# Performance work log

Measured on AMD Instinct MI355X. Metric: run time of the kernel, lower is better.

The kernel has to match this reference:

```python
import jax, jax.numpy as jnp
import numpy as np

N_NODES = 100000
IN_DIM = 64
OUT_DIM = 64
N_EDGES = 1250000


def setup_inputs() -> dict:
    key = jax.random.key(0)
    k1, k2, k3, k4 = jax.random.split(key, 4)
    x = jax.random.normal(k1, (N_NODES, IN_DIM), dtype=jnp.float32)
    edge_index = jax.random.randint(k2, (2, N_EDGES), 0, N_NODES, dtype=jnp.int32)
    # Linear weights stored as [in, out] so y = x @ W (equivalent to torch x @ W.T)
    s = 1.0 / np.sqrt(IN_DIM)
    W1 = jax.random.uniform(k3, (IN_DIM, OUT_DIM), dtype=jnp.float32, minval=-s, maxval=s)
    W2 = jax.random.uniform(k4, (IN_DIM, OUT_DIM), dtype=jnp.float32, minval=-s, maxval=s)
    return {"x": x, "edge_index": edge_index, "W1": W1, "W2": W2}


def reference(x, edge_index, W1, W2):
    # self part: [N, out]
    self_part = x @ W1
    # transform-then-gather is mathematically identical to gather-then-transform
    # (linear map commutes with row gather) and cheaper when E > N.
    msgs = (x @ W2)[edge_index[0]]            # [E, out]
    neighbor_part = jax.ops.segment_sum(msgs, edge_index[1], num_segments=x.shape[0])
    return jax.nn.relu(self_part + neighbor_part)
```

## Files before the change

kernel.cpp:

```cpp
#include <hip/hip_runtime.h>

#define N_NODES 100000
#define N_EDGES 1250000
#define DIM 64

#define B_SHIFT 7
#define BUCKET_NODES 128
#define NBUCKETS ((N_NODES + BUCKET_NODES - 1) / BUCKET_NODES)
#define CAP 2560
#define P_CHUNK 4096
#define P_THREADS 512
#define NBLK_P ((N_EDGES + P_CHUNK - 1) / P_CHUNK)
#define GEMM_BLOCKS 512
#define SG_THREADS 1024

typedef __attribute__((ext_vector_type(8))) short short8;
typedef __attribute__((ext_vector_type(4))) float f32x4;

static __host__ __device__ inline size_t align256(size_t x) { return (x + 255) & ~(size_t)255; }

__device__ inline float bf16_to_f32(unsigned short u) {
  return __uint_as_float(((unsigned)u) << 16);
}
__device__ inline unsigned short f32_to_bf16(float f) {
  unsigned u = __float_as_uint(f);
  u += 0x7FFFu + ((u >> 16) & 1u);
  return (unsigned short)(u >> 16);
}

__global__ __launch_bounds__(P_THREADS) void partition_sorted(
    const int* __restrict__ ei,
    int* __restrict__ gcursor,
    unsigned* __restrict__ pairs) {
  __shared__ int h[NBUCKETS];
  __shared__ int scn[NBUCKETS];
  __shared__ int cur[NBUCKETS];
  __shared__ int gbase[NBUCKETS];
  __shared__ int tsum[P_THREADS];
  __shared__ unsigned sval[P_CHUNK];
  __shared__ int saddr[P_CHUNK];

  const int nE = N_EDGES;
  int tid = threadIdx.x;
  int base = blockIdx.x * P_CHUNK;
  int end = min(base + P_CHUNK, nE);
  int cntE = end - base;

  for (int i = tid; i < NBUCKETS; i += P_THREADS) h[i] = 0;
  __syncthreads();
  for (int e = base + tid; e < end; e += P_THREADS)
    atomicAdd(&h[ei[nE + e] >> B_SHIFT], 1);
  __syncthreads();

  {
    int b0 = tid * 2;
    int l0 = 0, l1 = 0, s = 0;
    if (b0 < NBUCKETS)     { l0 = s; s += h[b0]; }
    if (b0 + 1 < NBUCKETS) { l1 = s; s += h[b0 + 1]; }
    tsum[tid] = s;
    __syncthreads();
    for (int off = 1; off < P_THREADS; off <<= 1) {
      int t = (tid >= off) ? tsum[tid - off] : 0;
      __syncthreads();
      tsum[tid] += t;
      __syncthreads();
    }
    int p = tsum[tid] - s;
    if (b0 < NBUCKETS)     scn[b0] = p + l0;
    if (b0 + 1 < NBUCKETS) scn[b0 + 1] = p + l1;
  }
  __syncthreads();

  for (int i = tid; i < NBUCKETS; i += P_THREADS) {
    int c = h[i];
    gbase[i] = c ? atomicAdd(&gcursor[i], c) : 0;
    cur[i] = scn[i];
  }
  __syncthreads();

  for (int e = base + tid; e < end; e += P_THREADS) {
    int dst = ei[nE + e];
    int src = ei[e];
    int b = dst >> B_SHIFT;
    int lp = atomicAdd(&cur[b], 1);
    int inb = lp - scn[b];
    int gpos = gbase[b] + inb;
    sval[lp] = (unsigned)src | ((unsigned)(dst & (BUCKET_NODES - 1)) << 17);
    saddr[lp] = (gpos < CAP) ? (b * CAP + gpos) : -1;
  }
  __syncthreads();

  for (int j = tid; j < cntE; j += P_THREADS) {
    int a = saddr[j];
    if (a >= 0) pairs[a] = sval[j];
  }
}

__global__ __launch_bounds__(256) void gemm_mfma(
    const float* __restrict__ x,
    const float* __restrict__ W1,
    const float* __restrict__ W2,
    unsigned short* __restrict__ y1b,
    unsigned short* __restrict__ y2b,
    int nTiles) {
  int lane = threadIdx.x & 63;
  int wave = (blockIdx.x * 256 + (int)threadIdx.x) >> 6;
  int nWaves = GEMM_BLOCKS * 4;
  int m = lane & 15;
  int q = lane >> 4;

  short8 wf[2][2][4];
#pragma unroll
  for (int w = 0; w < 2; ++w) {
    const float* W = w ? W2 : W1;
#pragma unroll
    for (int kh = 0; kh < 2; ++kh)
#pragma unroll
      for (int nt = 0; nt < 4; ++nt) {
        short8 f;
#pragma unroll
        for (int j = 0; j < 8; ++j) {
          int k = kh * 32 + q * 8 + j;
          f[j] = (short)f32_to_bf16(W[k * DIM + nt * 16 + m]);
        }
        wf[w][kh][nt] = f;
      }
  }

  for (int t = wave; t < nTiles; t += nWaves) {
    int rowBase = t * 16;
    const float* xr = x + (size_t)(rowBase + m) * DIM + q * 8;

    short8 af[2];
#pragma unroll
    for (int kh = 0; kh < 2; ++kh) {
      float4 u0 = *(const float4*)(xr + kh * 32);
      float4 u1 = *(const float4*)(xr + kh * 32 + 4);
      short8 f;
      f[0] = (short)f32_to_bf16(u0.x);
      f[1] = (short)f32_to_bf16(u0.y);
      f[2] = (short)f32_to_bf16(u0.z);
      f[3] = (short)f32_to_bf16(u0.w);
      f[4] = (short)f32_to_bf16(u1.x);
      f[5] = (short)f32_to_bf16(u1.y);
      f[6] = (short)f32_to_bf16(u1.z);
      f[7] = (short)f32_to_bf16(u1.w);
      af[kh] = f;
    }

#pragma unroll
    for (int w = 0; w < 2; ++w) {
      unsigned short* Y = w ? y2b : y1b;
      f32x4 acc[4];
#pragma unroll
      for (int nt = 0; nt < 4; ++nt) {
        acc[nt] = (f32x4){0.f, 0.f, 0.f, 0.f};
        acc[nt] = __builtin_amdgcn_mfma_f32_16x16x32_bf16(af[0], wf[w][0][nt], acc[nt], 0, 0, 0);
        acc[nt] = __builtin_amdgcn_mfma_f32_16x16x32_bf16(af[1], wf[w][1][nt], acc[nt], 0, 0, 0);
      }
#pragma unroll
      for (int nt = 0; nt < 4; ++nt)
#pragma unroll
        for (int r = 0; r < 4; ++r)
          Y[(size_t)(rowBase + q * 4 + r) * DIM + nt * 16 + m] = f32_to_bf16(acc[nt][r]);
    }
  }
}

__global__ __launch_bounds__(SG_THREADS) void sort_gather(
    const unsigned* __restrict__ pairs,
    const int* __restrict__ gcursor,
    const unsigned short* __restrict__ y1b,
    const unsigned short* __restrict__ y2b,
    float* __restrict__ out,
    int nNodesTotal) {
  __shared__ unsigned buf[CAP];
  __shared__ unsigned sorted[CAP];
  __shared__ int cnt[BUCKET_NODES];
  __shared__ int scn[BUCKET_NODES];
  __shared__ int cur[BUCKET_NODES];

  int b = blockIdx.x;
  int n = min(gcursor[b], CAP);
  int tid = threadIdx.x;
  const unsigned* pb = pairs + (size_t)b * CAP;

  if (tid < BUCKET_NODES) cnt[tid] = 0;
  __syncthreads();
  for (int i = tid; i < n; i += SG_THREADS) {
    unsigned w = pb[i];
    buf[i] = w;
    atomicAdd(&cnt[(w >> 17) & 127], 1);
  }
  __syncthreads();

  int v = 0;
  if (tid < BUCKET_NODES) { v = cnt[tid]; scn[tid] = v; }
  __syncthreads();
#pragma unroll
  for (int off = 1; off < BUCKET_NODES; off <<= 1) {
    int t = 0;
    if (tid < BUCKET_NODES && tid >= off) t = scn[tid - off];
    __syncthreads();
    if (tid < BUCKET_NODES) scn[tid] += t;
    __syncthreads();
  }
  if (tid < BUCKET_NODES) cur[tid] = scn[tid] - v;
  __syncthreads();

  for (int i = tid; i < n; i += SG_THREADS) {
    unsigned w = buf[i];
    int l = (int)((w >> 17) & 127);
    int p = atomicAdd(&cur[l], 1);
    sorted[p] = w & 0x1FFFFu;
  }
  __syncthreads();

  int lane = tid & 63;
  int wv = tid >> 6;
  int g = lane >> 4;
  int c16 = lane & 15;
  const ushort4* y2q = (const ushort4*)y2b;
  const ushort4* y1q = (const ushort4*)y1b;
  int nodeBase = b << B_SHIFT;
  int numNodes = min(BUCKET_NODES, nNodesTotal - nodeBase);

  for (int ln = wv; ln < numNodes; ln += (SG_THREADS / 64)) {
    int deg = cnt[ln];
    int begin = scn[ln] - deg;
    int end = begin + deg;

    float ax = 0.f, ay = 0.f, az = 0.f, aw = 0.f;
    float bx = 0.f, by = 0.f, bz = 0.f, bw = 0.f;
    int e = begin;
    for (; e + 7 < end; e += 8) {
      int s0 = (int)sorted[e + g];
      int s1 = (int)sorted[e + 4 + g];
      ushort4 u0 = y2q[(size_t)s0 * 16 + c16];
      ushort4 u1 = y2q[(size_t)s1 * 16 + c16];
      ax += bf16_to_f32(u0.x); ay += bf16_to_f32(u0.y);
      az += bf16_to_f32(u0.z); aw += bf16_to_f32(u0.w);
      bx += bf16_to_f32(u1.x); by += bf16_to_f32(u1.y);
      bz += bf16_to_f32(u1.z); bw += bf16_to_f32(u1.w);
    }
    for (; e + 3 < end; e += 4) {
      int s = (int)sorted[e + g];
      ushort4 u = y2q[(size_t)s * 16 + c16];
      ax += bf16_to_f32(u.x); ay += bf16_to_f32(u.y);
      az += bf16_to_f32(u.z); aw += bf16_to_f32(u.w);
    }
    if (e + g < end) {
      int s = (int)sorted[e + g];
      ushort4 u = y2q[(size_t)s * 16 + c16];
      ax += bf16_to_f32(u.x); ay += bf16_to_f32(u.y);
      az += bf16_to_f32(u.z); aw += bf16_to_f32(u.w);
    }

    float sx = ax + bx, sy = ay + by, sz = az + bz, sw = aw + bw;
    sx += __shfl_xor(sx, 16, 64);
    sy += __shfl_xor(sy, 16, 64);
    sz += __shfl_xor(sz, 16, 64);
    sw += __shfl_xor(sw, 16, 64);
    sx += __shfl_xor(sx, 32, 64);
    sy += __shfl_xor(sy, 32, 64);
    sz += __shfl_xor(sz, 32, 64);
    sw += __shfl_xor(sw, 32, 64);

    if (lane < 16) {
      int node = nodeBase + ln;
      ushort4 s1v = y1q[(size_t)node * 16 + lane];
      float4 o;
      o.x = fmaxf(bf16_to_f32(s1v.x) + sx, 0.0f);
      o.y = fmaxf(bf16_to_f32(s1v.y) + sy, 0.0f);
      o.z = fmaxf(bf16_to_f32(s1v.z) + sz, 0.0f);
      o.w = fmaxf(bf16_to_f32(s1v.w) + sw, 0.0f);
      ((float4*)out)[(size_t)node * 16 + lane] = o;
    }
  }
}

__global__ __launch_bounds__(256) void gemm_simple(
    const float* __restrict__ x, const float* __restrict__ W1, const float* __restrict__ W2,
    float* __restrict__ y1, unsigned short* __restrict__ y2b, int n) {
  int row = blockIdx.x * blockDim.x + threadIdx.x;
  if (row >= n) return;
  float xv[DIM];
  const float4* xr = (const float4*)(x + (size_t)row * DIM);
#pragma unroll
  for (int i = 0; i < DIM / 4; ++i) {
    float4 t = xr[i];
    xv[4 * i] = t.x; xv[4 * i + 1] = t.y; xv[4 * i + 2] = t.z; xv[4 * i + 3] = t.w;
  }
#pragma unroll
  for (int m = 0; m < 2; ++m) {
    const float* W = (m == 0) ? W1 : W2;
#pragma unroll
    for (int cc = 0; cc < DIM; cc += 16) {
      float acc[16];
#pragma unroll
      for (int c2 = 0; c2 < 16; ++c2) acc[c2] = 0.0f;
      for (int k = 0; k < DIM; ++k) {
        float xk = xv[k];
        const float* wr = W + k * DIM + cc;
#pragma unroll
        for (int c2 = 0; c2 < 16; ++c2) acc[c2] = fmaf(xk, wr[c2], acc[c2]);
      }
      if (m == 0) {
        for (int c2 = 0; c2 < 16; ++c2) y1[(size_t)row * DIM + cc + c2] = acc[c2];
      } else {
        for (int c2 = 0; c2 < 16; ++c2) y2b[(size_t)row * DIM + cc + c2] = f32_to_bf16(acc[c2]);
      }
    }
  }
}

__global__ __launch_bounds__(256) void scatter_add(const int* __restrict__ ei,
                                                   const unsigned short* __restrict__ y2b,
                                                   float* __restrict__ out, int nE) {
  int gid = blockIdx.x * blockDim.x + threadIdx.x;
  int edge = gid >> 6;
  int lane = threadIdx.x & 63;
  if (edge >= nE) return;
  int src = __builtin_amdgcn_readfirstlane(ei[edge]);
  int dst = __builtin_amdgcn_readfirstlane(ei[nE + edge]);
  atomicAdd(&out[(size_t)dst * DIM + lane], bf16_to_f32(y2b[(size_t)src * DIM + lane]));
}

__global__ __launch_bounds__(256) void relu_inplace(float* __restrict__ out, int n4) {
  int i = blockIdx.x * blockDim.x + threadIdx.x;
  if (i >= n4) return;
  float4* p = (float4*)out;
  float4 v = p[i];
  v.x = fmaxf(v.x, 0.0f);
  v.y = fmaxf(v.y, 0.0f);
  v.z = fmaxf(v.z, 0.0f);
  v.w = fmaxf(v.w, 0.0f);
  p[i] = v;
}

extern "C" void kernel_launch(void* const* d_in, const int* in_sizes, int n_in,
                              void* d_out, int out_size, void* d_ws, size_t ws_size,
                              hipStream_t stream) {
  const float* x  = (const float*)d_in[0];
  const int*   ei = (const int*)d_in[1];
  const float* W1 = (const float*)d_in[2];
  const float* W2 = (const float*)d_in[3];
  float* out = (float*)d_out;

  char* ws = (char*)d_ws;
  size_t off = 0;
  unsigned short* y2b = (unsigned short*)(ws + off); off += align256((size_t)N_NODES * DIM * sizeof(unsigned short));
  unsigned short* y1b = (unsigned short*)(ws + off); off += align256((size_t)N_NODES * DIM * sizeof(unsigned short));
  int* gcursor = (int*)(ws + off);                   off += align256((size_t)NBUCKETS * sizeof(int));
  unsigned* pairs = (unsigned*)(ws + off);           off += align256((size_t)NBUCKETS * CAP * sizeof(unsigned));
  size_t required = off;

  if (ws_size >= required) {
    hipMemsetAsync(gcursor, 0, (size_t)NBUCKETS * sizeof(int), stream);
    partition_sorted<<<NBLK_P, P_THREADS, 0, stream>>>(ei, gcursor, pairs);
    gemm_mfma<<<GEMM_BLOCKS, 256, 0, stream>>>(x, W1, W2, y1b, y2b, N_NODES / 16);
    sort_gather<<<NBUCKETS, SG_THREADS, 0, stream>>>(pairs, gcursor, y1b, y2b, out, N_NODES);
  } else {
    {
      int blocks = (N_NODES + 255) / 256;
      gemm_simple<<<blocks, 256, 0, stream>>>(x, W1, W2, out, y2b, N_NODES);
    }
    {
      long long threads = (long long)N_EDGES * 64;
      int blocks = (int)((threads + 255) / 256);
      scatter_add<<<blocks, 256, 0, stream>>>(ei, y2b, out, N_EDGES);
    }
    {
      int n4 = N_NODES * DIM / 4;
      int blocks = (n4 + 255) / 256;
      relu_inplace<<<blocks, 256, 0, stream>>>(out, n4);
    }
  }
}
```

Baseline: 148.7 us.

## Fuse GEMM and edge partition into one launch and use wave-shuffle scan

Merges the edge-partition kernel and the MFMA GEMM kernel into a single launch, with block index choosing which role a block plays, so the two independent stages can run concurrently and one launch gap goes away. GEMM blocks now use 512 threads and their count is halved, which keeps the total number of GEMM waves the same. Separately, the 128-entry scan in sort_gather now uses one wave with shuffle-up instead of a barrier-based shared-memory scan. The GEMM blocks now reserve the partition kernel's large shared-memory footprint, which may lower their occupancy.

```diff
diff --git a/kernel.cpp b/kernel.cpp
--- a/kernel.cpp
+++ b/kernel.cpp
@@ -11,7 +11,7 @@
 #define P_CHUNK 4096
 #define P_THREADS 512
 #define NBLK_P ((N_EDGES + P_CHUNK - 1) / P_CHUNK)
-#define GEMM_BLOCKS 512
+#define GEMM_BLOCKS 256
 #define SG_THREADS 1024
 
 typedef __attribute__((ext_vector_type(8))) short short8;
@@ -28,10 +28,16 @@
   return (unsigned short)(u >> 16);
 }
 
-__global__ __launch_bounds__(P_THREADS) void partition_sorted(
+__global__ __launch_bounds__(P_THREADS) void fused_gemm_partition(
+    const float* __restrict__ x,
+    const float* __restrict__ W1,
+    const float* __restrict__ W2,
+    unsigned short* __restrict__ y1b,
+    unsigned short* __restrict__ y2b,
     const int* __restrict__ ei,
     int* __restrict__ gcursor,
-    unsigned* __restrict__ pairs) {
+    unsigned* __restrict__ pairs,
+    int nTiles) {
   __shared__ int h[NBUCKETS];
   __shared__ int scn[NBUCKETS];
   __shared__ int cur[NBUCKETS];
@@ -40,129 +46,123 @@
   __shared__ unsigned sval[P_CHUNK];
   __shared__ int saddr[P_CHUNK];
 
-  const int nE = N_EDGES;
-  int tid = threadIdx.x;
-  int base = blockIdx.x * P_CHUNK;
-  int end = min(base + P_CHUNK, nE);
-  int cntE = end - base;
-
-  for (int i = tid; i < NBUCKETS; i += P_THREADS) h[i] = 0;
-  __syncthreads();
-  for (int e = base + tid; e < end; e += P_THREADS)
-    atomicAdd(&h[ei[nE + e] >> B_SHIFT], 1);
-  __syncthreads();
-
-  {
-    int b0 = tid * 2;
-    int l0 = 0, l1 = 0, s = 0;
-    if (b0 < NBUCKETS)     { l0 = s; s += h[b0]; }
-    if (b0 + 1 < NBUCKETS) { l1 = s; s += h[b0 + 1]; }
-    tsum[tid] = s;
-    __syncthreads();
-    for (int off = 1; off < P_THREADS; off <<= 1) {
-      int t = (tid >= off) ? tsum[tid - off] : 0;
+  if (blockIdx.x < NBLK_P) {
+    const int nE = N_EDGES;
+    int tid = threadIdx.x;
+    int base = blockIdx.x * P_CHUNK;
+    int end = min(base + P_CHUNK, nE);
+    int cntE = end - base;
+
+    for (int i = tid; i < NBUCKETS; i += P_THREADS) h[i] = 0;
+    __syncthreads();
+    for (int e = base + tid; e < end; e += P_THREADS)
+      atomicAdd(&h[ei[nE + e] >> B_SHIFT], 1);
+    __syncthreads();
+
+    {
+      int b0 = tid * 2;
+      int l0 = 0, l1 = 0, s = 0;
+      if (b0 < NBUCKETS)     { l0 = s; s += h[b0]; }
+      if (b0 + 1 < NBUCKETS) { l1 = s; s += h[b0 + 1]; }
+      tsum[tid] = s;
       __syncthreads();
-      tsum[tid] += t;
-      __syncthreads();
-    }
-    int p = tsum[tid] - s;
-    if (b0 < NBUCKETS)     scn[b0] = p + l0;
-    if (b0 + 1 < NBUCKETS) scn[b0 + 1] = p + l1;
-  }
-  __syncthreads();
-
-  for (int i = tid; i < NBUCKETS; i += P_THREADS) {
-    int c = h[i];
-    gbase[i] = c ? atomicAdd(&gcursor[i], c) : 0;
-    cur[i] = scn[i];
-  }
-  __syncthreads();
-
-  for (int e = base + tid; e < end; e += P_THREADS) {
-    int dst = ei[nE + e];
-    int src = ei[e];
-    int b = dst >> B_SHIFT;
-    int lp = atomicAdd(&cur[b], 1);
-    int inb = lp - scn[b];
-    int gpos = gbase[b] + inb;
-    sval[lp] = (unsigned)src | ((unsigned)(dst & (BUCKET_NODES - 1)) << 17);
-    saddr[lp] = (gpos < CAP) ? (b * CAP + gpos) : -1;
-  }
-  __syncthreads();
-
-  for (int j = tid; j < cntE; j += P_THREADS) {
-    int a = saddr[j];
-    if (a >= 0) pairs[a] = sval[j];
-  }
-}
-
-__global__ __launch_bounds__(256) void gemm_mfma(
-    const float* __restrict__ x,
-    const float* __restrict__ W1,
-    const float* __restrict__ W2,
-    unsigned short* __restrict__ y1b,
-    unsigned short* __restrict__ y2b,
-    int nTiles) {
-  int lane = threadIdx.x & 63;
-  int wave = (blockIdx.x * 256 + (int)threadIdx.x) >> 6;
-  int nWaves = GEMM_BLOCKS * 4;
-  int m = lane & 15;
-  int q = lane >> 4;
-
-  short8 wf[2][2][4];
-#pragma unroll
-  for (int w = 0; w < 2; ++w) {
-    const float* W = w ? W2 : W1;
-#pragma unroll
-    for (int kh = 0; kh < 2; ++kh)
-#pragma unroll
-      for (int nt = 0; nt < 4; ++nt) {
+      for (int off = 1; off < P_THREADS; off <<= 1) {
+        int t = (tid >= off) ? tsum[tid - off] : 0;
+        __syncthreads();
+        tsum[tid] += t;
+        __syncthreads();
+      }
+      int p = tsum[tid] - s;
+      if (b0 < NBUCKETS)     scn[b0] = p + l0;
+      if (b0 + 1 < NBUCKETS) scn[b0 + 1] = p + l1;
+    }
+    __syncthreads();
+
+    for (int i = tid; i < NBUCKETS; i += P_THREADS) {
+      int c = h[i];
+      gbase[i] = c ? atomicAdd(&gcursor[i], c) : 0;
+      cur[i] = scn[i];
+    }
+    __syncthreads();
+
+    for (int e = base + tid; e < end; e += P_THREADS) {
+      int dst = ei[nE + e];
+      int src = ei[e];
+      int b = dst >> B_SHIFT;
+      int lp = atomicAdd(&cur[b], 1);
+      int inb = lp - scn[b];
+      int gpos = gbase[b] + inb;
+      sval[lp] = (unsigned)src | ((unsigned)(dst & (BUCKET_NODES - 1)) << 17);
+      saddr[lp] = (gpos < CAP) ? (b * CAP + gpos) : -1;
+    }
+    __syncthreads();
+
+    for (int j = tid; j < cntE; j += P_THREADS) {
+      int a = saddr[j];
+      if (a >= 0) pairs[a] = sval[j];
+    }
+  } else {
+    int lane = threadIdx.x & 63;
+    int wave = ((blockIdx.x - NBLK_P) * P_THREADS + (int)threadIdx.x) >> 6;
+    int nWaves = GEMM_BLOCKS * (P_THREADS / 64);
+    int m = lane & 15;
+    int q = lane >> 4;
+
+    short8 wf[2][2][4];
+#pragma unroll
+    for (int w = 0; w < 2; ++w) {
+      const float* W = w ? W2 : W1;
+#pragma unroll
+      for (int kh = 0; kh < 2; ++kh)
+#pragma unroll
+        for (int nt = 0; nt < 4; ++nt) {
+          short8 f;
+#pragma unroll
+          for (int j = 0; j < 8; ++j) {
+            int k = kh * 32 + q * 8 + j;
+            f[j] = (short)f32_to_bf16(W[k * DIM + nt * 16 + m]);
+          }
+          wf[w][kh][nt] = f;
+        }
+    }
+
+    for (int t = wave; t < nTiles; t += nWaves) {
+      int rowBase = t * 16;
+      const float* xr = x + (size_t)(rowBase + m) * DIM + q * 8;
+
+      short8 af[2];
+#pragma unroll
+      for (int kh = 0; kh < 2; ++kh) {
+        float4 u0 = *(const float4*)(xr + kh * 32);
+        float4 u1 = *(const float4*)(xr + kh * 32 + 4);
         short8 f;
-#pragma unroll
-        for (int j = 0; j < 8; ++j) {
-          int k = kh * 32 + q * 8 + j;
-          f[j] = (short)f32_to_bf16(W[k * DIM + nt * 16 + m]);
+        f[0] = (short)f32_to_bf16(u0.x);
+        f[1] = (short)f32_to_bf16(u0.y);
+        f[2] = (short)f32_to_bf16(u0.z);
+        f[3] = (short)f32_to_bf16(u0.w);
+        f[4] = (short)f32_to_bf16(u1.x);
+        f[5] = (short)f32_to_bf16(u1.y);
+        f[6] = (short)f32_to_bf16(u1.z);
+        f[7] = (short)f32_to_bf16(u1.w);
+        af[kh] = f;
+      }
+
+#pragma unroll
+      for (int w = 0; w < 2; ++w) {
+        unsigned short* Y = w ? y2b : y1b;
+        f32x4 acc[4];
+#pragma unroll
+        for (int nt = 0; nt < 4; ++nt) {
+          acc[nt] = (f32x4){0.f, 0.f, 0.f, 0.f};
+          acc[nt] = __builtin_amdgcn_mfma_f32_16x16x32_bf16(af[0], wf[w][0][nt], acc[nt], 0, 0, 0);
+          acc[nt] = __builtin_amdgcn_mfma_f32_16x16x32_bf16(af[1], wf[w][1][nt], acc[nt], 0, 0, 0);
         }
-        wf[w][kh][nt] = f;
-      }
-  }
-
-  for (int t = wave; t < nTiles; t += nWaves) {
-    int rowBase = t * 16;
-    const float* xr = x + (size_t)(rowBase + m) * DIM + q * 8;
-
-    short8 af[2];
-#pragma unroll
-    for (int kh = 0; kh < 2; ++kh) {
-      float4 u0 = *(const float4*)(xr + kh * 32);
-      float4 u1 = *(const float4*)(xr + kh * 32 + 4);
-      short8 f;
-      f[0] = (short)f32_to_bf16(u0.x);
-      f[1] = (short)f32_to_bf16(u0.y);
-      f[2] = (short)f32_to_bf16(u0.z);
-      f[3] = (short)f32_to_bf16(u0.w);
-      f[4] = (short)f32_to_bf16(u1.x);
-      f[5] = (short)f32_to_bf16(u1.y);
-      f[6] = (short)f32_to_bf16(u1.z);
-      f[7] = (short)f32_to_bf16(u1.w);
-      af[kh] = f;
-    }
-
-#pragma unroll
-    for (int w = 0; w < 2; ++w) {
-      unsigned short* Y = w ? y2b : y1b;
-      f32x4 acc[4];
-#pragma unroll
-      for (int nt = 0; nt < 4; ++nt) {
-        acc[nt] = (f32x4){0.f, 0.f, 0.f, 0.f};
-        acc[nt] = __builtin_amdgcn_mfma_f32_16x16x32_bf16(af[0], wf[w][0][nt], acc[nt], 0, 0, 0);
-        acc[nt] = __builtin_amdgcn_mfma_f32_16x16x32_bf16(af[1], wf[w][1][nt], acc[nt], 0, 0, 0);
-      }
-#pragma unroll
-      for (int nt = 0; nt < 4; ++nt)
-#pragma unroll
-        for (int r = 0; r < 4; ++r)
-          Y[(size_t)(rowBase + q * 4 + r) * DIM + nt * 16 + m] = f32_to_bf16(acc[nt][r]);
+#pragma unroll
+        for (int nt = 0; nt < 4; ++nt)
+#pragma unroll
+          for (int r = 0; r < 4; ++r)
+            Y[(size_t)(rowBase + q * 4 + r) * DIM + nt * 16 + m] = f32_to_bf16(acc[nt][r]);
+      }
     }
   }
 }
@@ -194,18 +194,20 @@
   }
   __syncthreads();
 
-  int v = 0;
-  if (tid < BUCKET_NODES) { v = cnt[tid]; scn[tid] = v; }
-  __syncthreads();
-#pragma unroll
-  for (int off = 1; off < BUCKET_NODES; off <<= 1) {
-    int t = 0;
-    if (tid < BUCKET_NODES && tid >= off) t = scn[tid - off];
-    __syncthreads();
-    if (tid < BUCKET_NODES) scn[tid] += t;
-    __syncthreads();
-  }
-  if (tid < BUCKET_NODES) cur[tid] = scn[tid] - v;
+  if (tid < 64) {
+    int b0 = tid * 2;
+    int c0 = cnt[b0], c1 = cnt[b0 + 1];
+    int s = c0 + c1;
+#pragma unroll
+    for (int off = 1; off < 64; off <<= 1) {
+      int t = __shfl_up(s, off, 64);
+      if (tid >= off) s += t;
+    }
+    scn[b0] = s - c1;
+    scn[b0 + 1] = s;
+    cur[b0] = s - c1 - c0;
+    cur[b0 + 1] = s - c1;
+  }
   __syncthreads();
 
   for (int i = tid; i < n; i += SG_THREADS) {
@@ -357,8 +359,8 @@
 
   if (ws_size >= required) {
     hipMemsetAsync(gcursor, 0, (size_t)NBUCKETS * sizeof(int), stream);
-    partition_sorted<<<NBLK_P, P_THREADS, 0, stream>>>(ei, gcursor, pairs);
-    gemm_mfma<<<GEMM_BLOCKS, 256, 0, stream>>>(x, W1, W2, y1b, y2b, N_NODES / 16);
+    fused_gemm_partition<<<NBLK_P + GEMM_BLOCKS, P_THREADS, 0, stream>>>(
+        x, W1, W2, y1b, y2b, ei, gcursor, pairs, N_NODES / 16);
     sort_gather<<<NBUCKETS, SG_THREADS, 0, stream>>>(pairs, gcursor, y1b, y2b, out, N_NODES);
   } else {
     {
```

Measured after the change: 147.3 us. Within noise of the previous version (-0.9%).
